# Kernel optimization log

Hardware: AMD Instinct MI355X
Metric: run time of the kernel (lower is better)

Reference implementation:

```python
import jax, jax.numpy as jnp
import numpy as np

N_USERS = 100000
N_ITEMS = 50000
D = 128          # n_factors
L = 200          # hist_len
B = 2048
SIGMA = 0.1      # hyper_approx (posterior lognormal scale)
PRIOR = 1.0      # hyper_prior (prior lognormal scale)
TAU = 4.0
EPS = 1e-8
LN_EPS = 1e-5


def _layernorm(x, gamma, beta):
    m = jnp.mean(x, axis=-1, keepdims=True)
    v = jnp.var(x, axis=-1, keepdims=True)
    return (x - m) * jax.lax.rsqrt(v + LN_EPS) * gamma + beta


def setup_inputs() -> dict:
    key = jax.random.key(0)
    ks = jax.random.split(key, 20)
    user_idx = jax.random.randint(ks[0], (B,), 0, N_USERS, dtype=jnp.int32)
    item_idx = jax.random.randint(ks[1], (B,), 0, N_ITEMS, dtype=jnp.int32)
    # user_hist buffer: per-user ragged history padded with N_ITEMS
    lengths = jax.random.randint(ks[2], (N_USERS,), 1, L + 1, dtype=jnp.int32)
    raw_hist = jax.random.randint(ks[3], (N_USERS, L), 0, N_ITEMS, dtype=jnp.int32)
    pos = jnp.arange(L, dtype=jnp.int32)
    user_hist = jnp.where(pos[None, :] < lengths[:, None], raw_hist, N_ITEMS).astype(jnp.int32)
    # embeddings (padding rows zeroed, std=0.01 init)
    user_embed = 0.01 * jax.random.normal(ks[4], (N_USERS + 1, D), dtype=jnp.float32)
    user_embed = user_embed.at[N_USERS].set(0.0)
    item_embed = 0.01 * jax.random.normal(ks[5], (N_ITEMS + 1, D), dtype=jnp.float32)
    item_embed = item_embed.at[N_ITEMS].set(0.0)
    s = 1.0 / np.sqrt(D)
    W_i = s * jax.random.normal(ks[6], (D, D), dtype=jnp.float32)
    W_h = s * jax.random.normal(ks[7], (D, D), dtype=jnp.float32)
    # BAM 'concat' (additive) score params: v^T tanh(Wq q + Wk k)
    Wq = s * jax.random.normal(ks[8], (D, D), dtype=jnp.float32)
    Wk = s * jax.random.normal(ks[9], (D, D), dtype=jnp.float32)
    v_attn = s * jax.random.normal(ks[10], (D,), dtype=jnp.float32)
    pred_W = s * jax.random.normal(ks[11], (D,), dtype=jnp.float32)
    pred_b = jnp.zeros((), dtype=jnp.float32)
    gamma_u = jnp.ones((D,), jnp.float32); beta_u = jnp.zeros((D,), jnp.float32)
    gamma_i = jnp.ones((D,), jnp.float32); beta_i = jnp.zeros((D,), jnp.float32)
    # reparameterization noise (forward uses stochastic=True)
    noise_u = jax.random.normal(ks[12], (B, L), dtype=jnp.float32)
    noise_i = jax.random.normal(ks[13], (B, L), dtype=jnp.float32)
    return dict(user_idx=user_idx, item_idx=item_idx, user_hist=user_hist,
                user_embed=user_embed, item_embed=item_embed, W_i=W_i, W_h=W_h,
                Wq=Wq, Wk=Wk, v_attn=v_attn, pred_W=pred_W, pred_b=pred_b,
                gamma_u=gamma_u, beta_u=beta_u, gamma_i=gamma_i, beta_i=beta_i,
                noise_u=noise_u, noise_i=noise_i)


def reference(user_idx, item_idx, user_hist, user_embed, item_embed, W_i, W_h,
              Wq, Wk, v_attn, pred_W, pred_b, gamma_u, beta_u, gamma_i, beta_i,
              noise_u, noise_i):
    maskf_dummy = None  # (placeholder, no-op)
    hist = user_hist[user_idx]                                   # (B, L) int
    mask = (hist != item_idx[:, None]) & (hist != N_ITEMS)       # (B, L) bool
    maskf = mask.astype(jnp.float32)

    u_id = user_embed[user_idx]                                  # (B, D)
    t_raw = item_embed[item_idx]                                 # (B, D)
    h_raw = item_embed[hist]                                     # (B, L, D)
    t_id = t_raw @ W_i.T                                         # W_i(target)
    h_id = h_raw @ W_h.T                                         # W_h(hist)

    def bam(q, K, V, noise):
        # additive ('concat') scoring: v . tanh(q Wq + K Wk), temperature tau
        h = jnp.tanh((q @ Wq.T)[:, None, :] + jnp.einsum('bld,ed->ble', K, Wk))
        scores = jnp.einsum('ble,e->bl', h, v_attn) / TAU        # (B, L)
        scores = jnp.where(mask, scores, -1e9)
        phi = jax.nn.softmax(scores, axis=-1)                    # (B, L)
        mu = jnp.log(phi + EPS)
        w = jnp.exp(mu + SIGMA * noise) * maskf                  # lognormal sample
        attn = w / (jnp.sum(w, axis=-1, keepdims=True) + EPS)
        out = jnp.einsum('bl,bld->bd', attn, V)                  # (B, D)
        # KL( LN(mu, SIGMA) || LN(0, PRIOR) ) over valid positions
        kl_el = jnp.log(PRIOR / SIGMA) + (SIGMA ** 2 + mu ** 2) / (2.0 * PRIOR ** 2) - 0.5
        kl = jnp.sum(kl_el * maskf) / (jnp.sum(maskf) + EPS)
        return out, kl

    u_hist, kl_u = bam(u_id, h_id, h_id, noise_u)
    i_hist, kl_i = bam(t_id, h_id, h_id, noise_i)
    u = _layernorm(u_hist * u_id, gamma_u, beta_u)
    i = _layernorm(i_hist * t_id, gamma_i, beta_i)
    logit = (u * i) @ pred_W + pred_b                            # (B,)
    return logit, 0.5 * (kl_u + kl_i)
```

## Files before the change

### kernel.cpp

```cpp
#include <hip/hip_runtime.h>

#define B_ 2048
#define L_ 200
#define D_ 128
#define NITEMS 50000

typedef __attribute__((ext_vector_type(8))) short short8v;
typedef __attribute__((ext_vector_type(4))) float floatx4;
typedef __attribute__((ext_vector_type(4))) int intx4;

__device__ __forceinline__ short f2bf(float f) {
    union { float f; unsigned u; } v;
    v.f = f;
    unsigned r = v.u + 0x7FFFu + ((v.u >> 16) & 1u);
    return (short)(r >> 16);
}
__device__ __forceinline__ float bf2f(unsigned short s) {
    union { unsigned u; float f; } v;
    v.u = ((unsigned)s) << 16;
    return v.f;
}

__device__ __forceinline__ float tanh5(float x) {
    const float x2 = x * x;
    const float p = __builtin_fmaf(x2, 0.13333333f, -0.33333333f);
    return __builtin_fmaf(x * x2, p, x);
}

__device__ __forceinline__ float wave_sum(float v) {
#pragma unroll
    for (int m = 32; m >= 1; m >>= 1) v += __shfl_xor(v, m, 64);
    return v;
}

__device__ __forceinline__ void gload_lds16(const short* g, short* l) {
    __builtin_amdgcn_global_load_lds(
        (const __attribute__((address_space(1))) void*)g,
        (__attribute__((address_space(3))) void*)l, 16, 0, 0);
}

__device__ __forceinline__ intx4 ds_read16(const short* p) {
    intx4 d;
    asm volatile("ds_read_b128 %0, %1"
                 : "=v"(d)
                 : "v"((const __attribute__((address_space(3))) short*)p));
    return d;
}

__global__ __launch_bounds__(256) void k01(const float* __restrict__ Wk,
                                           const float* __restrict__ Wh,
                                           short* __restrict__ Mbf,
                                           const float* __restrict__ src,
                                           short* __restrict__ dst, int n8) {
    const int t = threadIdx.x;
    if (blockIdx.x < 128) {
        __shared__ float wk[128];
        const int e = blockIdx.x;
        if (t < 128) wk[t] = Wk[e * 128 + t];
        __syncthreads();
        if (t < 128) {
            float s = 0.f;
#pragma unroll 4
            for (int d = 0; d < 128; ++d) s += wk[d] * Wh[d * 128 + t];
            Mbf[e * 128 + t] = f2bf(s);
        }
        return;
    }
    const int i = (blockIdx.x - 128) * 256 + t;
    if (i >= n8) return;
    const float4 f0 = *reinterpret_cast<const float4*>(src + i * 8);
    const float4 f1 = *reinterpret_cast<const float4*>(src + i * 8 + 4);
    short8v w;
    w[0] = f2bf(f0.x); w[1] = f2bf(f0.y); w[2] = f2bf(f0.z); w[3] = f2bf(f0.w);
    w[4] = f2bf(f1.x); w[5] = f2bf(f1.y); w[6] = f2bf(f1.z); w[7] = f2bf(f1.w);
    *reinterpret_cast<short8v*>(dst + i * 8) = w;
}

__global__ __launch_bounds__(256) void k2_prep(
    const int* __restrict__ user_idx, const int* __restrict__ item_idx,
    const int* __restrict__ user_hist, const float* __restrict__ user_embed,
    const float* __restrict__ item_embed, const float* __restrict__ W_i,
    const float* __restrict__ Wq, float* __restrict__ uid_o,
    float* __restrict__ tid_o, float* __restrict__ qu_o, float* __restrict__ qt_o,
    int* __restrict__ hist_o) {
    const int bb = blockIdx.x * 4, t = threadIdx.x;
    __shared__ float uid_s[4][128], traw_s[4][128], tid_s[4][128];
    __shared__ int uis[4], iis[4];
    if (t < 4) {
        uis[t] = user_idx[bb + t];
        iis[t] = item_idx[bb + t];
    }
    __syncthreads();
#pragma unroll
    for (int c = 0; c < 2; ++c) {
        const int idx = c * 256 + t;
        const int bs = idx >> 7, e = idx & 127;
        const float uv = user_embed[(long)uis[bs] * 128 + e];
        uid_s[bs][e] = uv;
        traw_s[bs][e] = item_embed[(long)iis[bs] * 128 + e];
        uid_o[(bb + bs) * 128 + e] = uv;
    }
    for (int l0 = t; l0 < 800; l0 += 256) {
        const int bs = (l0 >= 200) + (l0 >= 400) + (l0 >= 600);
        hist_o[bb * 200 + l0] = user_hist[(long)uis[bs] * 200 + (l0 - bs * 200)];
    }
    __syncthreads();
    {
        const int half = t >> 7, e = t & 127;
        const float* Wrow = (half ? Wq : W_i) + e * 128;
        float acc[4] = {0.f, 0.f, 0.f, 0.f};
        for (int c = 0; c < 128; c += 4) {
            const float4 w = *reinterpret_cast<const float4*>(Wrow + c);
#pragma unroll
            for (int k = 0; k < 4; ++k) {
                const float4 s = half ? *reinterpret_cast<const float4*>(&uid_s[k][c])
                                      : *reinterpret_cast<const float4*>(&traw_s[k][c]);
                acc[k] += w.x * s.x + w.y * s.y + w.z * s.z + w.w * s.w;
            }
        }
#pragma unroll
        for (int k = 0; k < 4; ++k) {
            if (half) qu_o[(bb + k) * 128 + e] = acc[k];
            else {
                tid_s[k][e] = acc[k];
                tid_o[(bb + k) * 128 + e] = acc[k];
            }
        }
    }
    __syncthreads();
    {
        const int half = t >> 7, e = t & 127;
        const float* Wrow = Wq + e * 128;
        float acc[2] = {0.f, 0.f};
        for (int c = 0; c < 128; c += 4) {
            const float4 w = *reinterpret_cast<const float4*>(Wrow + c);
#pragma unroll
            for (int k = 0; k < 2; ++k) {
                const float4 s = *reinterpret_cast<const float4*>(&tid_s[half * 2 + k][c]);
                acc[k] += w.x * s.x + w.y * s.y + w.z * s.z + w.w * s.w;
            }
        }
#pragma unroll
        for (int k = 0; k < 2; ++k) qt_o[(bb + half * 2 + k) * 128 + e] = acc[k];
    }
}

__global__ __launch_bounds__(512) void k345(
    const short* __restrict__ Mbf, const short* __restrict__ item_bf,
    const int* __restrict__ hist_g, const int* __restrict__ item_idx,
    const float* __restrict__ qu_, const float* __restrict__ qt_,
    const float* __restrict__ v_attn, const float* __restrict__ noise_u,
    const float* __restrict__ noise_i, const float* __restrict__ W_h,
    const float* __restrict__ uid, const float* __restrict__ tid,
    const float* __restrict__ gamma_u, const float* __restrict__ beta_u,
    const float* __restrict__ gamma_i, const float* __restrict__ beta_i,
    const float* __restrict__ pred_W, const float* __restrict__ pred_b,
    float* __restrict__ klu, float* __restrict__ kli, float* __restrict__ msm,
    float* __restrict__ out) {
    __shared__ __align__(16) short M_lds[8][4][4][16][8];
    __shared__ __align__(16) char scratch[16384];
    __shared__ float q_lds[2][2][128];
    __shared__ float v_lds[128];
    __shared__ unsigned short hgs[400];
    __shared__ unsigned short scA[800];
    __shared__ float red[8];

    const int t = threadIdx.x, blk = blockIdx.x;
    const int b0 = blk * 2;
    const int ii0 = item_idx[b0], ii1 = item_idx[b0 + 1];

#pragma unroll
    for (int c4 = 0; c4 < 4; ++c4) {
        const int flat = c4 * 512 + t;
        const int lo2 = flat & 15, g = (flat >> 4) & 3, ks = (flat >> 6) & 3, t8 = flat >> 8;
        *reinterpret_cast<short8v*>(&M_lds[t8][ks][g][lo2][0]) =
            *reinterpret_cast<const short8v*>(Mbf + (t8 * 16 + lo2) * 128 + ks * 32 + g * 8);
    }
    {
        const int bs = t >> 8, side = (t >> 7) & 1, e = t & 127;
        q_lds[bs][side][e] =
            side ? qt_[(b0 + bs) * 128 + e] : qu_[(b0 + bs) * 128 + e];
    }
    if (t < 128) v_lds[t] = v_attn[t];
    if (t < 400) hgs[t] = (unsigned short)hist_g[blk * 400 + t];
    __syncthreads();

    const int wid = t >> 6, lane = t & 63;
    const int lo = lane & 15, hi = lane >> 4;

    {
        const int nt = (wid == 7) ? 4 : 3;
        short* wbase = reinterpret_cast<short*>(scratch) + wid * 1024;
        const char* itemc = (const char*)item_bf;

        int ro[4];
#pragma unroll
        for (int i = 0; i < 4; ++i) {
            const int lt = min(wid * 3 + ((i < 3) ? i : 3), 24);
            ro[i] = (int)hgs[lt * 16 + lo];
        }
        auto stage_half = [&](int i, int h) {
            const char* rp = itemc + ((long)ro[i] << 8) + hi * 16 + h * 128;
            gload_lds16((const short*)rp, wbase);
            gload_lds16((const short*)(rp + 64), wbase + 512);
        };

        stage_half(0, 0);
        for (int i = 0; i < nt; ++i) {
            floatx4 acc[8];
#pragma unroll
            for (int t8 = 0; t8 < 8; ++t8) acc[t8] = (floatx4){0.f, 0.f, 0.f, 0.f};
            const short* pb = wbase + hi * 128 + lo * 8;

            asm volatile("s_waitcnt vmcnt(0)" ::: "memory");
            __builtin_amdgcn_sched_barrier(0);
            intx4 r0 = ds_read16(pb);
            intx4 r1 = ds_read16(pb + 512);
            asm volatile("s_waitcnt lgkmcnt(0)" ::: "memory");
            __builtin_amdgcn_sched_barrier(0);
            short8v f0 = __builtin_bit_cast(short8v, r0);
            short8v f1 = __builtin_bit_cast(short8v, r1);
            stage_half(i, 1);
            __builtin_amdgcn_sched_barrier(0);
#pragma unroll
            for (int t8 = 0; t8 < 8; ++t8)
                acc[t8] = __builtin_amdgcn_mfma_f32_16x16x32_bf16(
                    *reinterpret_cast<const short8v*>(&M_lds[t8][0][hi][lo][0]), f0,
                    acc[t8], 0, 0, 0);
#pragma unroll
            for (int t8 = 0; t8 < 8; ++t8)
                acc[t8] = __builtin_amdgcn_mfma_f32_16x16x32_bf16(
                    *reinterpret_cast<const short8v*>(&M_lds[t8][1][hi][lo][0]), f1,
                    acc[t8], 0, 0, 0);

            asm volatile("s_waitcnt vmcnt(0)" ::: "memory");
            __builtin_amdgcn_sched_barrier(0);
            intx4 r2 = ds_read16(pb);
            intx4 r3 = ds_read16(pb + 512);
            asm volatile("s_waitcnt lgkmcnt(0)" ::: "memory");
            __builtin_amdgcn_sched_barrier(0);
            short8v f2 = __builtin_bit_cast(short8v, r2);
            short8v f3 = __builtin_bit_cast(short8v, r3);
            if (i + 1 < nt) stage_half(i + 1, 0);
            __builtin_amdgcn_sched_barrier(0);
#pragma unroll
            for (int t8 = 0; t8 < 8; ++t8)
                acc[t8] = __builtin_amdgcn_mfma_f32_16x16x32_bf16(
                    *reinterpret_cast<const short8v*>(&M_lds[t8][2][hi][lo][0]), f2,
                    acc[t8], 0, 0, 0);
#pragma unroll
            for (int t8 = 0; t8 < 8; ++t8)
                acc[t8] = __builtin_amdgcn_mfma_f32_16x16x32_bf16(
                    *reinterpret_cast<const short8v*>(&M_lds[t8][3][hi][lo][0]), f3,
                    acc[t8], 0, 0, 0);

            const int lr = (wid * 3 + i) * 16 + lo;
            const int bs = lr >= 200;
            float su = 0.f, si = 0.f;
#pragma unroll
            for (int t8 = 0; t8 < 8; ++t8) {
                const floatx4 vv = *reinterpret_cast<const floatx4*>(&v_lds[t8 * 16 + hi * 4]);
                const floatx4 qa = *reinterpret_cast<const floatx4*>(&q_lds[bs][0][t8 * 16 + hi * 4]);
                const floatx4 qb = *reinterpret_cast<const floatx4*>(&q_lds[bs][1][t8 * 16 + hi * 4]);
#pragma unroll
                for (int rg = 0; rg < 4; ++rg) {
                    su = __builtin_fmaf(vv[rg], tanh5(qa[rg] + acc[t8][rg]), su);
                    si = __builtin_fmaf(vv[rg], tanh5(qb[rg] + acc[t8][rg]), si);
                }
            }
            su += __shfl_xor(su, 16, 64);
            su += __shfl_xor(su, 32, 64);
            si += __shfl_xor(si, 16, 64);
            si += __shfl_xor(si, 32, 64);
            if (hi == 0) {
                scA[lr] = (unsigned short)f2bf(su * 0.25f);
                scA[400 + lr] = (unsigned short)f2bf(si * 0.25f);
            }
        }
    }
    __syncthreads();

    if (wid < 4) {
        const int bs = wid & 1, side = wid >> 1;
        const int bb = b0 + bs;
        const int iiv = bs ? ii1 : ii0;
        const float* nz = (side ? noise_i : noise_u) + bb * L_;
        unsigned short* scl = scA + side * 400 + bs * 200;
        const unsigned short* hrow = hgs + bs * 200;

        float mk[4], s2[4];
        float msl = 0.f, esum = 0.f;
#pragma unroll
        for (int k = 0; k < 4; ++k) {
            const int l = lane + 64 * k;
            const int hv = (l < L_) ? (int)hrow[l] : NITEMS;
            mk[k] = (l < L_ && hv != iiv && hv != NITEMS) ? 1.f : 0.f;
            msl += mk[k];
            const float s = (mk[k] > 0.5f) ? bf2f(scl[(l < L_) ? l : 0]) : -1e9f;
            s2[k] = s * 1.4426950f;
            esum += exp2f(s2[k]);
        }
        const float msum = wave_sum(msl);
        float Z = wave_sum(esum);
        Z = fmaxf(Z, 1e-37f);
        const float z2 = log2f(Z);

        float wv[4], wsum = 0.f, klsum = 0.f;
#pragma unroll
        for (int k = 0; k < 4; ++k) {
            const int l = lane + 64 * k;
            const int lm = (l < L_) ? l : 0;
            const float d = s2[k] - z2;
            wv[k] = exp2f(__builtin_fmaf(nz[lm], 0.14426950f, d)) * mk[k];
            wsum += wv[k];
            klsum += (1.8075851f + 0.2402265f * d * d) * mk[k];
        }
        const float Zw = wave_sum(wsum);
        const float kls = wave_sum(klsum);
        const float invZw = 1.f / (Zw + 1e-8f);
#pragma unroll
        for (int k = 0; k < 4; ++k) {
            const int l = lane + 64 * k;
            if (l < L_) scl[l] = (unsigned short)f2bf(wv[k] * invZw);
        }
        if (lane == 0) {
            if (side == 0) { klu[bb] = kls; msm[bb] = msum; }
            else kli[bb] = kls;
        }
    }
    __syncthreads();

    float* P = reinterpret_cast<float*>(scratch);
    {
        const int bs = wid >> 2, rg = wid & 3, c2 = lane;
        const unsigned short* a0p = scA + bs * 200;
        const unsigned short* a1p = scA + 400 + bs * 200;
        const unsigned short* hrow = hgs + bs * 200;
        float s00 = 0.f, s01 = 0.f, s10 = 0.f, s11 = 0.f;
#pragma unroll
        for (int c = 0; c < 2; ++c) {
            const int lb = rg * 50 + c * 25;
            unsigned hv[25];
#pragma unroll
            for (int j = 0; j < 25; ++j)
                hv[j] = *reinterpret_cast<const unsigned*>(
                    item_bf + (long)hrow[lb + j] * 128 + c2 * 2);
#pragma unroll
            for (int j = 0; j < 25; ++j) {
                const float h0 = __uint_as_float(hv[j] << 16);
                const float h1 = __uint_as_float(hv[j] & 0xffff0000u);
                const float a0 = bf2f(a0p[lb + j]);
                const float a1 = bf2f(a1p[lb + j]);
                s00 += a0 * h0; s01 += a0 * h1;
                s10 += a1 * h0; s11 += a1 * h1;
            }
        }
        P[((bs * 2 + 0) * 4 + rg) * 128 + c2 * 2] = s00;
        P[((bs * 2 + 0) * 4 + rg) * 128 + c2 * 2 + 1] = s01;
        P[((bs * 2 + 1) * 4 + rg) * 128 + c2 * 2] = s10;
        P[((bs * 2 + 1) * 4 + rg) * 128 + c2 * 2 + 1] = s11;
    }
    __syncthreads();

    const int bs3 = t >> 8, side3 = (t >> 7) & 1, tl = t & 127;
    const int grp = t >> 7;
    {
        const int gidx = (bs3 * 2 + side3) * 4;
        float a = P[(gidx + 0) * 128 + tl] + P[(gidx + 1) * 128 + tl] +
                  P[(gidx + 2) * 128 + tl] + P[(gidx + 3) * 128 + tl];
        __syncthreads();
        P[2048 + grp * 128 + tl] = a;
    }
    __syncthreads();

    float x;
    {
        const float* vsrc = P + 2048 + grp * 128;
        float o = 0.f;
#pragma unroll 2
        for (int c = 0; c < 128; c += 4) {
            const float4 w = *reinterpret_cast<const float4*>(&W_h[tl * 128 + c]);
            o += w.x * vsrc[c] + w.y * vsrc[c + 1] + w.z * vsrc[c + 2] + w.w * vsrc[c + 3];
        }
        x = o * (side3 ? tid[(b0 + bs3) * 128 + tl] : uid[(b0 + bs3) * 128 + tl]);
    }
    const float v1 = wave_sum(x);
    if (lane == 0) red[wid] = v1;
    __syncthreads();
    const float mean = (red[grp * 2] + red[grp * 2 + 1]) * (1.f / 128.f);
    const float d = x - mean;
    const float v2 = wave_sum(d * d);
    __syncthreads();
    if (lane == 0) red[wid] = v2;
    __syncthreads();
    const float var = (red[grp * 2] + red[grp * 2 + 1]) * (1.f / 128.f);
    const float gmm = side3 ? gamma_i[tl] : gamma_u[tl];
    const float bta = side3 ? beta_i[tl] : beta_u[tl];
    const float uin = d * rsqrtf(var + 1e-5f) * gmm + bta;
    __syncthreads();
    P[2560 + grp * 128 + tl] = uin;
    __syncthreads();
    float p = 0.f;
    if (t < 256) {
        const int bs = t >> 7, tl2 = t & 127;
        p = P[2560 + (bs * 2 + 0) * 128 + tl2] * P[2560 + (bs * 2 + 1) * 128 + tl2] *
            pred_W[tl2];
    }
    const float v3 = wave_sum(p);
    if (lane == 0 && wid < 4) red[4 + wid] = v3;
    __syncthreads();
    if (t == 0) out[b0] = red[4] + red[5] + pred_b[0];
    if (t == 1) out[b0 + 1] = red[6] + red[7] + pred_b[0];
}

__global__ __launch_bounds__(256) void k6_kl(const float* __restrict__ klu,
                                             const float* __restrict__ kli,
                                             const float* __restrict__ msm,
                                             float* __restrict__ out) {
    __shared__ float red[4];
    const int t = threadIdx.x;
    float su = 0.f, si = 0.f, sm = 0.f;
    for (int b = t; b < B_; b += 256) {
        su += klu[b];
        si += kli[b];
        sm += msm[b];
    }
    su = wave_sum(su);
    si = wave_sum(si);
    sm = wave_sum(sm);
    __syncthreads();
    if ((t & 63) == 0) red[t >> 6] = su;
    __syncthreads();
    su = red[0] + red[1] + red[2] + red[3];
    __syncthreads();
    if ((t & 63) == 0) red[t >> 6] = si;
    __syncthreads();
    si = red[0] + red[1] + red[2] + red[3];
    __syncthreads();
    if ((t & 63) == 0) red[t >> 6] = sm;
    __syncthreads();
    sm = red[0] + red[1] + red[2] + red[3];
    if (t == 0) {
        const float inv = 1.f / (sm + 1e-8f);
        out[0] = 0.5f * (su * inv + si * inv);
    }
}

extern "C" void kernel_launch(void* const* d_in, const int* in_sizes, int n_in,
                              void* d_out, int out_size, void* d_ws, size_t ws_size,
                              hipStream_t stream) {
    const int* user_idx = (const int*)d_in[0];
    const int* item_idx = (const int*)d_in[1];
    const int* user_hist = (const int*)d_in[2];
    const float* user_embed = (const float*)d_in[3];
    const float* item_embed = (const float*)d_in[4];
    const float* W_i = (const float*)d_in[5];
    const float* W_h = (const float*)d_in[6];
    const float* Wq = (const float*)d_in[7];
    const float* Wk = (const float*)d_in[8];
    const float* v_attn = (const float*)d_in[9];
    const float* pred_W = (const float*)d_in[10];
    const float* pred_b = (const float*)d_in[11];
    const float* gamma_u = (const float*)d_in[12];
    const float* beta_u = (const float*)d_in[13];
    const float* gamma_i = (const float*)d_in[14];
    const float* beta_i = (const float*)d_in[15];
    const float* noise_u = (const float*)d_in[16];
    const float* noise_i = (const float*)d_in[17];
    float* out = (float*)d_out;

    char* ws = (char*)d_ws;
    size_t off = 0;
    auto alloc = [&](size_t bytes) -> void* {
        void* p = ws + off;
        off = (off + bytes + 255) & ~(size_t)255;
        return p;
    };
    short* Mbf     = (short*)alloc(128 * 128 * 2);
    short* item_bf = (short*)alloc((size_t)(NITEMS + 1) * 128 * 2);
    float* uid = (float*)alloc((size_t)B_ * 128 * 4);
    float* tid = (float*)alloc((size_t)B_ * 128 * 4);
    float* qu  = (float*)alloc((size_t)B_ * 128 * 4);
    float* qt  = (float*)alloc((size_t)B_ * 128 * 4);
    int* hg    = (int*)alloc((size_t)B_ * L_ * 4);
    float* klu = (float*)alloc((size_t)B_ * 4);
    float* kli = (float*)alloc((size_t)B_ * 4);
    float* msm = (float*)alloc((size_t)B_ * 4);

    const int n8 = (NITEMS + 1) * 128 / 8;
    const int ncvt = (n8 + 255) / 256;
    k01<<<128 + ncvt, 256, 0, stream>>>(Wk, W_h, Mbf, item_embed, item_bf, n8);
    k2_prep<<<B_ / 4, 256, 0, stream>>>(user_idx, item_idx, user_hist, user_embed,
                                        item_embed, W_i, Wq, uid, tid, qu, qt, hg);
    k345<<<B_ / 2, 512, 0, stream>>>(Mbf, item_bf, hg, item_idx, qu, qt, v_attn,
                                     noise_u, noise_i, W_h, uid, tid, gamma_u, beta_u,
                                     gamma_i, beta_i, pred_W, pred_b, klu, kli, msm, out);
    k6_kl<<<1, 256, 0, stream>>>(klu, kli, msm, out + B_);
}
```

Baseline: 105.7 us.

## Process four batch rows per 1024-thread block in fused attention kernel

The fused attention kernel now handles four batch elements per block with 1024 threads instead of two with 512. Each block still loads the 32KB bf16 Wk matrix into LDS once, so the per-block setup cost is spread over twice as many rows. The 16 waves split the 50 row tiles unevenly (3 or 4 tiles each), and the shared scratch and scratch buffers are doubled in size. This costs higher LDS use per block and heavier register limits from the 1024-thread launch bounds, which may reduce occupancy.

```diff
diff --git a/kernel.cpp b/kernel.cpp
--- a/kernel.cpp
+++ b/kernel.cpp
@@ -145,7 +145,7 @@
     }
 }
 
-__global__ __launch_bounds__(512) void k345(
+__global__ __launch_bounds__(1024, 8) void k345(
     const short* __restrict__ Mbf, const short* __restrict__ item_bf,
     const int* __restrict__ hist_g, const int* __restrict__ item_idx,
     const float* __restrict__ qu_, const float* __restrict__ qt_,
@@ -158,20 +158,19 @@
     float* __restrict__ klu, float* __restrict__ kli, float* __restrict__ msm,
     float* __restrict__ out) {
     __shared__ __align__(16) short M_lds[8][4][4][16][8];
-    __shared__ __align__(16) char scratch[16384];
-    __shared__ float q_lds[2][2][128];
+    __shared__ __align__(16) char scratch[32768];
+    __shared__ float q_lds[4][2][128];
     __shared__ float v_lds[128];
-    __shared__ unsigned short hgs[400];
-    __shared__ unsigned short scA[800];
-    __shared__ float red[8];
+    __shared__ unsigned short hgs[800];
+    __shared__ unsigned short scA[1600];
+    __shared__ float red[16];
 
     const int t = threadIdx.x, blk = blockIdx.x;
-    const int b0 = blk * 2;
-    const int ii0 = item_idx[b0], ii1 = item_idx[b0 + 1];
-
-#pragma unroll
-    for (int c4 = 0; c4 < 4; ++c4) {
-        const int flat = c4 * 512 + t;
+    const int b0 = blk * 4;
+
+#pragma unroll
+    for (int c2 = 0; c2 < 2; ++c2) {
+        const int flat = c2 * 1024 + t;
         const int lo2 = flat & 15, g = (flat >> 4) & 3, ks = (flat >> 6) & 3, t8 = flat >> 8;
         *reinterpret_cast<short8v*>(&M_lds[t8][ks][g][lo2][0]) =
             *reinterpret_cast<const short8v*>(Mbf + (t8 * 16 + lo2) * 128 + ks * 32 + g * 8);
@@ -182,23 +181,22 @@
             side ? qt_[(b0 + bs) * 128 + e] : qu_[(b0 + bs) * 128 + e];
     }
     if (t < 128) v_lds[t] = v_attn[t];
-    if (t < 400) hgs[t] = (unsigned short)hist_g[blk * 400 + t];
+    if (t < 800) hgs[t] = (unsigned short)hist_g[blk * 800 + t];
     __syncthreads();
 
     const int wid = t >> 6, lane = t & 63;
     const int lo = lane & 15, hi = lane >> 4;
 
     {
-        const int nt = (wid == 7) ? 4 : 3;
+        const int tstart = (wid * 25) >> 3;
+        const int nt = (((wid + 1) * 25) >> 3) - tstart;
         short* wbase = reinterpret_cast<short*>(scratch) + wid * 1024;
         const char* itemc = (const char*)item_bf;
 
         int ro[4];
 #pragma unroll
-        for (int i = 0; i < 4; ++i) {
-            const int lt = min(wid * 3 + ((i < 3) ? i : 3), 24);
-            ro[i] = (int)hgs[lt * 16 + lo];
-        }
+        for (int i = 0; i < 4; ++i) ro[i] = (int)hgs[min(tstart + i, 49) * 16 + lo];
+
         auto stage_half = [&](int i, int h) {
             const char* rp = itemc + ((long)ro[i] << 8) + hi * 16 + h * 128;
             gload_lds16((const short*)rp, wbase);
@@ -254,8 +252,9 @@
                     *reinterpret_cast<const short8v*>(&M_lds[t8][3][hi][lo][0]), f3,
                     acc[t8], 0, 0, 0);
 
-            const int lr = (wid * 3 + i) * 16 + lo;
-            const int bs = lr >= 200;
+            const int lr = (tstart + i) * 16 + lo;
+            const int bs = (lr >= 200) + (lr >= 400) + (lr >= 600);
+            const int lb = lr - bs * 200;
             float su = 0.f, si = 0.f;
 #pragma unroll
             for (int t8 = 0; t8 < 8; ++t8) {
@@ -273,19 +272,19 @@
             si += __shfl_xor(si, 16, 64);
             si += __shfl_xor(si, 32, 64);
             if (hi == 0) {
-                scA[lr] = (unsigned short)f2bf(su * 0.25f);
-                scA[400 + lr] = (unsigned short)f2bf(si * 0.25f);
-            }
-        }
-    }
-    __syncthreads();
-
-    if (wid < 4) {
-        const int bs = wid & 1, side = wid >> 1;
+                scA[(bs * 2 + 0) * 200 + lb] = (unsigned short)f2bf(su * 0.25f);
+                scA[(bs * 2 + 1) * 200 + lb] = (unsigned short)f2bf(si * 0.25f);
+            }
+        }
+    }
+    __syncthreads();
+
+    if (wid < 8) {
+        const int side = wid & 1, bs = wid >> 1;
         const int bb = b0 + bs;
-        const int iiv = bs ? ii1 : ii0;
+        const int iiv = item_idx[bb];
         const float* nz = (side ? noise_i : noise_u) + bb * L_;
-        unsigned short* scl = scA + side * 400 + bs * 200;
+        unsigned short* scl = scA + (bs * 2 + side) * 200;
         const unsigned short* hrow = hgs + bs * 200;
 
         float mk[4], s2[4];
@@ -333,8 +332,8 @@
     float* P = reinterpret_cast<float*>(scratch);
     {
         const int bs = wid >> 2, rg = wid & 3, c2 = lane;
-        const unsigned short* a0p = scA + bs * 200;
-        const unsigned short* a1p = scA + 400 + bs * 200;
+        const unsigned short* a0p = scA + (bs * 2 + 0) * 200;
+        const unsigned short* a1p = scA + (bs * 2 + 1) * 200;
         const unsigned short* hrow = hgs + bs * 200;
         float s00 = 0.f, s01 = 0.f, s10 = 0.f, s11 = 0.f;
 #pragma unroll
@@ -362,20 +361,18 @@
     }
     __syncthreads();
 
-    const int bs3 = t >> 8, side3 = (t >> 7) & 1, tl = t & 127;
-    const int grp = t >> 7;
-    {
-        const int gidx = (bs3 * 2 + side3) * 4;
-        float a = P[(gidx + 0) * 128 + tl] + P[(gidx + 1) * 128 + tl] +
-                  P[(gidx + 2) * 128 + tl] + P[(gidx + 3) * 128 + tl];
-        __syncthreads();
-        P[2048 + grp * 128 + tl] = a;
+    const int grp = t >> 7, tl = t & 127;
+    const int bs3 = grp >> 1, side3 = grp & 1;
+    {
+        const float a = P[(grp * 4 + 0) * 128 + tl] + P[(grp * 4 + 1) * 128 + tl] +
+                        P[(grp * 4 + 2) * 128 + tl] + P[(grp * 4 + 3) * 128 + tl];
+        P[4096 + grp * 128 + tl] = a;
     }
     __syncthreads();
 
     float x;
     {
-        const float* vsrc = P + 2048 + grp * 128;
+        const float* vsrc = P + 4096 + grp * 128;
         float o = 0.f;
 #pragma unroll 2
         for (int c = 0; c < 128; c += 4) {
@@ -398,19 +395,18 @@
     const float bta = side3 ? beta_i[tl] : beta_u[tl];
     const float uin = d * rsqrtf(var + 1e-5f) * gmm + bta;
     __syncthreads();
-    P[2560 + grp * 128 + tl] = uin;
+    P[5120 + grp * 128 + tl] = uin;
     __syncthreads();
     float p = 0.f;
-    if (t < 256) {
-        const int bs = t >> 7, tl2 = t & 127;
-        p = P[2560 + (bs * 2 + 0) * 128 + tl2] * P[2560 + (bs * 2 + 1) * 128 + tl2] *
-            pred_W[tl2];
+    if (t < 512) {
+        const int bsl = t >> 7, tll = t & 127;
+        p = P[5120 + (bsl * 2 + 0) * 128 + tll] * P[5120 + (bsl * 2 + 1) * 128 + tll] *
+            pred_W[tll];
     }
     const float v3 = wave_sum(p);
-    if (lane == 0 && wid < 4) red[4 + wid] = v3;
-    __syncthreads();
-    if (t == 0) out[b0] = red[4] + red[5] + pred_b[0];
-    if (t == 1) out[b0 + 1] = red[6] + red[7] + pred_b[0];
+    if (lane == 0 && wid < 8) red[8 + wid] = v3;
+    __syncthreads();
+    if (t < 4) out[b0 + t] = red[8 + t * 2] + red[8 + t * 2 + 1] + pred_b[0];
 }
 
 __global__ __launch_bounds__(256) void k6_kl(const float* __restrict__ klu,
@@ -492,8 +488,8 @@
     k01<<<128 + ncvt, 256, 0, stream>>>(Wk, W_h, Mbf, item_embed, item_bf, n8);
     k2_prep<<<B_ / 4, 256, 0, stream>>>(user_idx, item_idx, user_hist, user_embed,
                                         item_embed, W_i, Wq, uid, tid, qu, qt, hg);
-    k345<<<B_ / 2, 512, 0, stream>>>(Mbf, item_bf, hg, item_idx, qu, qt, v_attn,
-                                     noise_u, noise_i, W_h, uid, tid, gamma_u, beta_u,
-                                     gamma_i, beta_i, pred_W, pred_b, klu, kli, msm, out);
+    k345<<<B_ / 4, 1024, 0, stream>>>(Mbf, item_bf, hg, item_idx, qu, qt, v_attn,
+                                      noise_u, noise_i, W_h, uid, tid, gamma_u, beta_u,
+                                      gamma_i, beta_i, pred_W, pred_b, klu, kli, msm, out);
     k6_kl<<<1, 256, 0, stream>>>(klu, kli, msm, out + B_);
 }
```

Measured after the change: 121.9 us. +15.3%, slower.
